# Kernel tuning notes

Measured on AMD Instinct MI355X. Metric: run time of the kernel, lower is better.

## Reference

```python
import jax, jax.numpy as jnp
import numpy as np

ALPHA = 0.05  # mixprop alpha
GDEP = 2      # propagation depth

B, C_IN, N, T = 2, 16, 4096, 12
C_OUT = 16


def _row_norm_with_self_loop(A):
    # A <- (A + I); A / rowsum(A)
    A = A + jnp.eye(A.shape[0], dtype=A.dtype)
    return A / A.sum(axis=1, keepdims=True)


def _qadj_mul(Ar, Ai, Aj, Ak, x):
    # quaternion Hamilton product of adjacency quaternion (Ar,Ai,Aj,Ak)
    # with feature quaternion (channel dim split into 4 components).
    # x: [b, c, n, t] with c % 4 == 0
    xr, xi, xj, xk = jnp.split(x, 4, axis=1)  # each [b, c/4, n, t]
    mm = lambda A, v: jnp.einsum('vw,bcwt->bcvt', A, v)
    out_r = mm(Ar, xr) - mm(Ai, xi) - mm(Aj, xj) - mm(Ak, xk)
    out_i = mm(Ar, xi) + mm(Ai, xr) + mm(Aj, xk) - mm(Ak, xj)
    out_j = mm(Ar, xj) - mm(Ai, xk) + mm(Aj, xr) + mm(Ak, xi)
    out_k = mm(Ar, xk) + mm(Ai, xj) - mm(Aj, xi) + mm(Ak, xr)
    return jnp.concatenate([out_r, out_i, out_j, out_k], axis=1)


def _make_quaternion_mul(kernel):
    # kernel: [K, c_in//4, c_out] -> hamilton: [K, c_in, c_out]
    r, i, j, k = jnp.split(kernel, 4, axis=2)  # each [K, c_in//4, c_out//4]
    r2 = jnp.concatenate([r, -i, -j, -k], axis=1)
    i2 = jnp.concatenate([i, r, -k, j], axis=1)
    j2 = jnp.concatenate([j, k, r, -i], axis=1)
    k2 = jnp.concatenate([k, -j, i, r], axis=1)
    return jnp.concatenate([r2, i2, j2, k2], axis=2)  # [K, c_in, c_out]


def setup_inputs() -> dict:
    key = jax.random.key(0)
    ks = jax.random.split(key, 6)
    x = jax.random.normal(ks[0], (B, C_IN, N, T), dtype=jnp.float32)
    adp_r = jax.random.uniform(ks[1], (N, N), dtype=jnp.float32)
    adp_i = jax.random.uniform(ks[2], (N, N), dtype=jnp.float32)
    adp_j = jax.random.uniform(ks[3], (N, N), dtype=jnp.float32)
    adp_k = jax.random.uniform(ks[4], (N, N), dtype=jnp.float32)
    weight = jax.random.normal(ks[5], (GDEP + 1, C_IN // 4, C_OUT), dtype=jnp.float32)
    return {"x": x, "adp_r": adp_r, "adp_i": adp_i, "adp_j": adp_j,
            "adp_k": adp_k, "weight": weight}


def reference(x, adp_r, adp_i, adp_j, adp_k, weight):
    a_r = adp_r  # note: r-component is NOT normalized in the original
    a_i = _row_norm_with_self_loop(adp_i)
    a_j = _row_norm_with_self_loop(adp_j)
    a_k = _row_norm_with_self_loop(adp_k)

    h = x
    out = [h]
    for _ in range(GDEP):
        h = ALPHA * x + (1.0 - ALPHA) * _qadj_mul(a_r, a_i, a_j, a_k, h)
        out.append(h)
    xs = jnp.stack(out, axis=2)  # [b, c_in, gdep+1, n, t]

    hamilton = _make_quaternion_mul(weight)  # [gdep+1, c_in, c_out]
    return jnp.einsum('bikht,kij->bjht', xs, hamilton)  # [b, c_out, n, t]
```

## Files before the change

### kernel.cpp

```cpp
#include <hip/hip_runtime.h>

typedef __attribute__((ext_vector_type(8))) short short8;
typedef __attribute__((ext_vector_type(4))) float f32x4;

#define ALPHA_F 0.05f

static __device__ __forceinline__ unsigned short f2bf(float f) {
  unsigned int u = __float_as_uint(f);
  unsigned int r = (u + 0x7fffu + ((u >> 16) & 1u)) >> 16;
  return (unsigned short)r;
}

static __device__ __forceinline__ void gld16(const void* g, void* l) {
  __builtin_amdgcn_global_load_lds((const __attribute__((address_space(1))) void*)g,
                                   (__attribute__((address_space(3))) void*)l, 16, 0, 0);
}

__global__ __launch_bounds__(256) void prep_adj(const float* __restrict__ ar,
    const float* __restrict__ ai, const float* __restrict__ aj, const float* __restrict__ ak,
    unsigned short* __restrict__ Abf)
{
  const int bid = blockIdx.x;
  const int p = bid >> 12;
  const int row = bid & 4095;
  const float* src = (p == 0) ? ar : (p == 1) ? ai : (p == 2) ? aj : ak;
  const float4* r4 = (const float4*)(src + ((size_t)row << 12));
  ushort4* dst = (ushort4*)(Abf + (((size_t)p << 12) + (size_t)row) * 4096);

  if (p == 0) {
    for (int i = threadIdx.x; i < 1024; i += 256) {
      float4 v = r4[i];
      dst[i] = make_ushort4(f2bf(v.x), f2bf(v.y), f2bf(v.z), f2bf(v.w));
    }
  } else {
    float4 vals[4];
    float s = 0.f;
    #pragma unroll
    for (int it = 0; it < 4; ++it) {
      float4 v = r4[threadIdx.x + it * 256];
      vals[it] = v;
      s += v.x + v.y + v.z + v.w;
    }
    #pragma unroll
    for (int off = 32; off >= 1; off >>= 1) s += __shfl_down(s, off, 64);
    __shared__ float red[4];
    if ((threadIdx.x & 63) == 0) red[threadIdx.x >> 6] = s;
    __syncthreads();
    const float inv = 1.0f / (red[0] + red[1] + red[2] + red[3] + 1.0f);
    #pragma unroll
    for (int it = 0; it < 4; ++it) {
      const int i = threadIdx.x + it * 256;
      float4 v = vals[it];
      const int base = i << 2;
      if (row - base >= 0 && row - base < 4) ((float*)&v)[row - base] += 1.0f;
      dst[i] = make_ushort4(f2bf(v.x * inv), f2bf(v.y * inv), f2bf(v.z * inv), f2bf(v.w * inv));
    }
  }
}

__global__ __launch_bounds__(256) void pack_x(const float* __restrict__ x,
                                              unsigned short* __restrict__ XT)
{
  __shared__ float tile[3072];
  const int nt = blockIdx.x & 15;
  const int c  = (blockIdx.x >> 4) & 15;
  const int b  = blockIdx.x >> 8;
  const int n0 = nt << 8;
  const int col0 = c * 24 + b * 12;
  const size_t base = ((size_t)(b * 16 + c) * 4096 + n0) * 12;
  #pragma unroll
  for (int it = 0; it < 12; ++it) {
    const int idx = it * 256 + threadIdx.x;
    tile[idx] = x[base + idx];
  }
  __syncthreads();
  #pragma unroll
  for (int it = 0; it < 12; ++it) {
    const int idx = it * 256 + threadIdx.x;
    const int t = idx >> 8, i = idx & 255;
    XT[(size_t)(col0 + t) * 4096 + (n0 + i)] = f2bf(tile[i * 12 + t]);
  }
}

#define SBM 64
#define SBN 384
#define SBK 64

__global__ __launch_bounds__(512, 2) void gemm_p(const unsigned short* __restrict__ A,
    const unsigned short* __restrict__ BT, float* __restrict__ P)
{
  __shared__ __align__(16) unsigned short As[2][SBM * SBK];
  __shared__ __align__(16) unsigned short Bs[2][SBN * SBK];
  const int tid = threadIdx.x;
  const int p  = blockIdx.x >> 6;
  const int n0 = (blockIdx.x & 63) << 6;
  const int lane = tid & 63;
  const int w = tid >> 6;
  const int wm = w >> 2;
  const int ws = w & 3;

  f32x4 acc[2][6];
  #pragma unroll
  for (int m = 0; m < 2; ++m)
    #pragma unroll
    for (int n = 0; n < 6; ++n) acc[m][n] = (f32x4){0.f, 0.f, 0.f, 0.f};

  auto stage = [&](int buf, int kt) {
    const int k0 = kt << 6;
    #pragma unroll
    for (int it = 0; it < 7; ++it) {
      const int idx = it * 512 + tid;
      if (it == 0) {
        const int row = idx >> 3, ch = idx & 7;
        const int chs = ch ^ (row & 7);
        gld16(A + (((size_t)(p * 4096 + n0 + row)) << 12) + (size_t)(k0 + chs * 8),
              (unsigned short*)As[buf] + idx * 8);
      } else {
        const int bidx = idx - 512;
        const int row = bidx >> 3, ch = bidx & 7;
        const int chs = ch ^ (row & 7);
        gld16(BT + ((size_t)row << 12) + (size_t)(k0 + chs * 8),
              (unsigned short*)Bs[buf] + bidx * 8);
      }
    }
  };

  stage(0, 0);
  const int l15 = lane & 15, lk = lane >> 4;
  const int NK = 64;
  for (int kt = 0; kt < NK; ++kt) {
    const int buf = kt & 1;
    if (kt + 1 < NK) {
      stage(buf ^ 1, kt + 1);
      asm volatile("s_waitcnt vmcnt(7)" ::: "memory");
    } else {
      asm volatile("s_waitcnt vmcnt(0)" ::: "memory");
    }
    __builtin_amdgcn_s_barrier();
    __builtin_amdgcn_sched_barrier(0);

    short8 af[2][2], bf[6][2];
    #pragma unroll
    for (int m = 0; m < 2; ++m) {
      const int row = wm * 32 + m * 16 + l15;
      #pragma unroll
      for (int ks = 0; ks < 2; ++ks) {
        const int ck = (lk + ks * 4) ^ (row & 7);
        af[m][ks] = *(const short8*)&As[buf][row * 64 + ck * 8];
      }
    }
    #pragma unroll
    for (int n = 0; n < 6; ++n) {
      const int row = ws * 96 + n * 16 + l15;
      #pragma unroll
      for (int ks = 0; ks < 2; ++ks) {
        const int ck = (lk + ks * 4) ^ (row & 7);
        bf[n][ks] = *(const short8*)&Bs[buf][row * 64 + ck * 8];
      }
    }
    __builtin_amdgcn_s_setprio(1);
    #pragma unroll
    for (int ks = 0; ks < 2; ++ks)
      #pragma unroll
      for (int m = 0; m < 2; ++m)
        #pragma unroll
        for (int n = 0; n < 6; ++n)
          acc[m][n] = __builtin_amdgcn_mfma_f32_16x16x32_bf16(af[m][ks], bf[n][ks], acc[m][n], 0, 0, 0);
    __builtin_amdgcn_s_setprio(0);
    __builtin_amdgcn_sched_barrier(0);
    __builtin_amdgcn_s_barrier();
  }

  float* Pp = P + ((size_t)p * 4096 + (size_t)n0) * 384;
  #pragma unroll
  for (int m = 0; m < 2; ++m) {
    const int r0 = wm * 32 + m * 16 + ((lane >> 4) << 2);
    #pragma unroll
    for (int n = 0; n < 6; ++n) {
      const int cc = ws * 96 + n * 16 + (lane & 15);
      #pragma unroll
      for (int e = 0; e < 4; ++e)
        Pp[(size_t)(r0 + e) * 384 + cc] = acc[m][n][e];
    }
  }
}

__global__ __launch_bounds__(256) void combine_k(const float* __restrict__ P,
    const float* __restrict__ x, float* __restrict__ H, unsigned short* __restrict__ XT,
    const int writeXT)
{
  __shared__ unsigned short T[64][72];
  const int n0 = (blockIdx.x / 6) << 6;
  const int c0 = (blockIdx.x % 6) << 6;
  static const int   sigma_t[4][4] = {{0,1,2,3},{1,0,3,2},{2,3,0,1},{3,2,1,0}};
  static const float sgn_t[4][4]   = {{1,-1,-1,-1},{1,1,1,-1},{1,-1,1,1},{1,1,-1,1}};
  #pragma unroll
  for (int r = 0; r < 16; ++r) {
    const int idx = r * 256 + threadIdx.x;
    const int ln = idx >> 6, lc = idx & 63;
    const int n = n0 + ln, col = c0 + lc;
    const int q = col / 96;
    const int cm = col - q * 96;
    float acc = 0.f;
    #pragma unroll
    for (int p = 0; p < 4; ++p)
      acc += sgn_t[q][p] * P[((size_t)p * 4096 + (size_t)n) * 384 + (size_t)(sigma_t[q][p] * 96 + cm)];
    const int c = col / 24, rr = col - c * 24;
    const int b = rr / 12, t = rr - b * 12;
    const float xv = x[(((size_t)(b * 16 + c) << 12) | (size_t)n) * 12 + t];
    const float h = ALPHA_F * xv + (1.f - ALPHA_F) * acc;
    H[(size_t)n * 384 + col] = h;
    T[lc][ln] = f2bf(h);
  }
  if (writeXT) {
    __syncthreads();
    #pragma unroll
    for (int r = 0; r < 16; ++r) {
      const int idx = r * 256 + threadIdx.x;
      const int lc = idx >> 6, ln = idx & 63;
      XT[((size_t)(c0 + lc) << 12) + (size_t)(n0 + ln)] = T[lc][ln];
    }
  }
}

__global__ __launch_bounds__(256) void final_k(const float* __restrict__ x,
    const float* __restrict__ H1, const float* __restrict__ H2,
    const float* __restrict__ wgt, float* __restrict__ out)
{
  __shared__ float Hm[3][16][16];
  static const int   comp_t[4][4] = {{0,1,2,3},{1,0,3,2},{2,3,0,1},{3,2,1,0}};
  static const float hsgn_t[4][4] = {{1,-1,-1,-1},{1,1,-1,1},{1,1,1,-1},{1,-1,1,1}};
  for (int idx = threadIdx.x; idx < 768; idx += 256) {
    const int k = idx >> 8, i = (idx >> 4) & 15, j = idx & 15;
    const int J = j >> 2, I = i >> 2, a = i & 3, jj = j & 3;
    Hm[k][i][j] = hsgn_t[J][I] * wgt[(k * 4 + a) * 16 + comp_t[J][I] * 4 + jj];
  }
  __syncthreads();
  const int o = blockIdx.x * 256 + threadIdx.x;
  const int t = o % 12;
  const int nb = o / 12;
  const int n = nb & 4095;
  const int b = nb >> 12;
  float v[3][16];
  #pragma unroll
  for (int i = 0; i < 16; ++i)
    v[0][i] = x[((((size_t)(b * 16 + i)) << 12) | (size_t)n) * 12 + t];
  const int colbase = b * 12 + t;
  #pragma unroll
  for (int i = 0; i < 16; ++i) {
    const size_t hidx = (size_t)n * 384 + (size_t)(i * 24 + colbase);
    v[1][i] = H1[hidx];
    v[2][i] = H2[hidx];
  }
  #pragma unroll
  for (int j = 0; j < 16; ++j) {
    float acc = 0.f;
    #pragma unroll
    for (int k = 0; k < 3; ++k)
      #pragma unroll
      for (int i = 0; i < 16; ++i)
        acc += v[k][i] * Hm[k][i][j];
    out[((((size_t)(b * 16 + j)) << 12) | (size_t)n) * 12 + t] = acc;
  }
}

extern "C" void kernel_launch(void* const* d_in, const int* in_sizes, int n_in,
                              void* d_out, int out_size, void* d_ws, size_t ws_size,
                              hipStream_t stream)
{
  const float* x   = (const float*)d_in[0];
  const float* ar  = (const float*)d_in[1];
  const float* ai  = (const float*)d_in[2];
  const float* aj  = (const float*)d_in[3];
  const float* ak  = (const float*)d_in[4];
  const float* wgt = (const float*)d_in[5];
  float* out = (float*)d_out;

  char* ws = (char*)d_ws;
  unsigned short* Abf = (unsigned short*)(ws);
  unsigned short* XT0 = (unsigned short*)(ws + 134217728);
  unsigned short* XT1 = (unsigned short*)(ws + 137363456);
  float*          P   = (float*)(ws + 140509184);
  float*          H1  = (float*)(ws + 165675008);
  float*          H2  = (float*)(ws + 171966464);

  prep_adj<<<dim3(16384), dim3(256), 0, stream>>>(ar, ai, aj, ak, Abf);
  pack_x<<<dim3(512), dim3(256), 0, stream>>>(x, XT0);
  gemm_p<<<dim3(256), dim3(512), 0, stream>>>(Abf, XT0, P);
  combine_k<<<dim3(384), dim3(256), 0, stream>>>(P, x, H1, XT1, 1);
  gemm_p<<<dim3(256), dim3(512), 0, stream>>>(Abf, XT1, P);
  combine_k<<<dim3(384), dim3(256), 0, stream>>>(P, x, H2, XT1, 0);
  final_k<<<dim3(384), dim3(256), 0, stream>>>(x, H1, H2, wgt, out);
}
```

Baseline: 506.9 us.

## Split-K GEMM with 128x192 tiles and one-wave-per-row adjacency prep

The adjacency GEMM is retiled from 64x384 blocks to 128x192 output tiles with a 2-way split over K, giving 512 blocks instead of 256 for better occupancy. Partial sums go to a doubled P buffer that combine_k now reduces over 8 slices, and the workspace offsets are shifted to make room. prep_adj assigns one wavefront per row and uses shuffle-xor reductions instead of block-level LDS reductions. The costs are extra P traffic, the split-K reduction, and some duplicated B loads from clamped rows.

Result: slower. 591.4 us (+16.7%).

```diff
diff --git a/kernel.cpp b/kernel.cpp
--- a/kernel.cpp
+++ b/kernel.cpp
@@ -20,41 +20,41 @@
     const float* __restrict__ ai, const float* __restrict__ aj, const float* __restrict__ ak,
     unsigned short* __restrict__ Abf)
 {
-  const int bid = blockIdx.x;
-  const int p = bid >> 12;
-  const int row = bid & 4095;
+  const int w = threadIdx.x >> 6, lane = threadIdx.x & 63;
+  const int wid = blockIdx.x * 4 + w;
+  const int p = wid >> 12;
+  const int row = wid & 4095;
   const float* src = (p == 0) ? ar : (p == 1) ? ai : (p == 2) ? aj : ak;
   const float4* r4 = (const float4*)(src + ((size_t)row << 12));
-  ushort4* dst = (ushort4*)(Abf + (((size_t)p << 12) + (size_t)row) * 4096);
+  ushort4* dst = (ushort4*)(Abf + ((size_t)wid << 12));
+
+  float4 v[16];
+  #pragma unroll
+  for (int i = 0; i < 16; ++i) v[i] = r4[lane + i * 64];
 
   if (p == 0) {
-    for (int i = threadIdx.x; i < 1024; i += 256) {
-      float4 v = r4[i];
-      dst[i] = make_ushort4(f2bf(v.x), f2bf(v.y), f2bf(v.z), f2bf(v.w));
-    }
+    #pragma unroll
+    for (int i = 0; i < 16; ++i)
+      dst[lane + i * 64] = make_ushort4(f2bf(v[i].x), f2bf(v[i].y), f2bf(v[i].z), f2bf(v[i].w));
   } else {
-    float4 vals[4];
     float s = 0.f;
     #pragma unroll
-    for (int it = 0; it < 4; ++it) {
-      float4 v = r4[threadIdx.x + it * 256];
-      vals[it] = v;
-      s += v.x + v.y + v.z + v.w;
-    }
-    #pragma unroll
-    for (int off = 32; off >= 1; off >>= 1) s += __shfl_down(s, off, 64);
-    __shared__ float red[4];
-    if ((threadIdx.x & 63) == 0) red[threadIdx.x >> 6] = s;
-    __syncthreads();
-    const float inv = 1.0f / (red[0] + red[1] + red[2] + red[3] + 1.0f);
-    #pragma unroll
-    for (int it = 0; it < 4; ++it) {
-      const int i = threadIdx.x + it * 256;
-      float4 v = vals[it];
-      const int base = i << 2;
-      if (row - base >= 0 && row - base < 4) ((float*)&v)[row - base] += 1.0f;
-      dst[i] = make_ushort4(f2bf(v.x * inv), f2bf(v.y * inv), f2bf(v.z * inv), f2bf(v.w * inv));
-    }
+    for (int i = 0; i < 16; ++i) s += v[i].x + v[i].y + v[i].z + v[i].w;
+    #pragma unroll
+    for (int off = 1; off < 64; off <<= 1) s += __shfl_xor(s, off, 64);
+    const float inv = 1.0f / (s + 1.0f);
+    #pragma unroll
+    for (int i = 0; i < 16; ++i) {
+      const int base = (i * 64 + lane) << 2;
+      v[i].x += (base + 0 == row) ? 1.0f : 0.0f;
+      v[i].y += (base + 1 == row) ? 1.0f : 0.0f;
+      v[i].z += (base + 2 == row) ? 1.0f : 0.0f;
+      v[i].w += (base + 3 == row) ? 1.0f : 0.0f;
+    }
+    #pragma unroll
+    for (int i = 0; i < 16; ++i)
+      dst[lane + i * 64] = make_ushort4(f2bf(v[i].x * inv), f2bf(v[i].y * inv),
+                                        f2bf(v[i].z * inv), f2bf(v[i].w * inv));
   }
 }
 
@@ -82,46 +82,44 @@
   }
 }
 
-#define SBM 64
-#define SBN 384
-#define SBK 64
-
-__global__ __launch_bounds__(512, 2) void gemm_p(const unsigned short* __restrict__ A,
+__global__ __launch_bounds__(512, 4) void gemm_p(const unsigned short* __restrict__ A,
     const unsigned short* __restrict__ BT, float* __restrict__ P)
 {
-  __shared__ __align__(16) unsigned short As[2][SBM * SBK];
-  __shared__ __align__(16) unsigned short Bs[2][SBN * SBK];
+  __shared__ __align__(16) unsigned short As[2][512 * 8];
+  __shared__ __align__(16) unsigned short Bs[2][1024 * 8];
   const int tid = threadIdx.x;
-  const int p  = blockIdx.x >> 6;
-  const int n0 = (blockIdx.x & 63) << 6;
+  const int bx = blockIdx.x;
+  const int p  = bx & 3;
+  const int nt = (bx >> 2) & 1;
+  const int kh = (bx >> 3) & 1;
+  const int m0 = (bx >> 4) << 7;
+  const int n0 = nt * 192;
+  const int kbase = kh * 2048;
   const int lane = tid & 63;
   const int w = tid >> 6;
   const int wm = w >> 2;
   const int ws = w & 3;
 
-  f32x4 acc[2][6];
-  #pragma unroll
-  for (int m = 0; m < 2; ++m)
-    #pragma unroll
-    for (int n = 0; n < 6; ++n) acc[m][n] = (f32x4){0.f, 0.f, 0.f, 0.f};
+  f32x4 acc[4][3];
+  #pragma unroll
+  for (int m = 0; m < 4; ++m)
+    #pragma unroll
+    for (int n = 0; n < 3; ++n) acc[m][n] = (f32x4){0.f, 0.f, 0.f, 0.f};
 
   auto stage = [&](int buf, int kt) {
-    const int k0 = kt << 6;
-    #pragma unroll
-    for (int it = 0; it < 7; ++it) {
-      const int idx = it * 512 + tid;
-      if (it == 0) {
-        const int row = idx >> 3, ch = idx & 7;
-        const int chs = ch ^ (row & 7);
-        gld16(A + (((size_t)(p * 4096 + n0 + row)) << 12) + (size_t)(k0 + chs * 8),
-              (unsigned short*)As[buf] + idx * 8);
-      } else {
-        const int bidx = idx - 512;
-        const int row = bidx >> 3, ch = bidx & 7;
-        const int chs = ch ^ (row & 7);
-        gld16(BT + ((size_t)row << 12) + (size_t)(k0 + chs * 8),
-              (unsigned short*)Bs[buf] + bidx * 8);
-      }
+    const int k0 = kbase + (kt << 5);
+    {
+      const int row = tid & 127, ch = tid >> 7;
+      gld16(A + (((size_t)(p * 4096 + m0 + row)) << 12) + (size_t)(k0 + ch * 8),
+            (unsigned short*)As[buf] + tid * 8);
+    }
+    #pragma unroll
+    for (int it = 0; it < 2; ++it) {
+      const int bidx = it * 512 + tid;
+      const int row = bidx & 255, ch = bidx >> 8;
+      const int grow = n0 + (row < 192 ? row : 191);
+      gld16(BT + ((size_t)grow << 12) + (size_t)(k0 + ch * 8),
+            (unsigned short*)Bs[buf] + bidx * 8);
     }
   };
 
@@ -132,52 +130,42 @@
     const int buf = kt & 1;
     if (kt + 1 < NK) {
       stage(buf ^ 1, kt + 1);
-      asm volatile("s_waitcnt vmcnt(7)" ::: "memory");
+      asm volatile("s_waitcnt vmcnt(3)" ::: "memory");
     } else {
       asm volatile("s_waitcnt vmcnt(0)" ::: "memory");
     }
     __builtin_amdgcn_s_barrier();
     __builtin_amdgcn_sched_barrier(0);
 
-    short8 af[2][2], bf[6][2];
-    #pragma unroll
-    for (int m = 0; m < 2; ++m) {
-      const int row = wm * 32 + m * 16 + l15;
+    short8 af[4], bfr[3];
+    #pragma unroll
+    for (int m = 0; m < 4; ++m) {
+      const int row = wm * 64 + m * 16 + l15;
+      af[m] = *(const short8*)&As[buf][(lk * 128 + row) * 8];
+    }
+    #pragma unroll
+    for (int n = 0; n < 3; ++n) {
+      const int row = ws * 48 + n * 16 + l15;
+      bfr[n] = *(const short8*)&Bs[buf][(lk * 256 + row) * 8];
+    }
+    __builtin_amdgcn_s_setprio(1);
+    #pragma unroll
+    for (int m = 0; m < 4; ++m)
       #pragma unroll
-      for (int ks = 0; ks < 2; ++ks) {
-        const int ck = (lk + ks * 4) ^ (row & 7);
-        af[m][ks] = *(const short8*)&As[buf][row * 64 + ck * 8];
-      }
-    }
-    #pragma unroll
-    for (int n = 0; n < 6; ++n) {
-      const int row = ws * 96 + n * 16 + l15;
-      #pragma unroll
-      for (int ks = 0; ks < 2; ++ks) {
-        const int ck = (lk + ks * 4) ^ (row & 7);
-        bf[n][ks] = *(const short8*)&Bs[buf][row * 64 + ck * 8];
-      }
-    }
-    __builtin_amdgcn_s_setprio(1);
-    #pragma unroll
-    for (int ks = 0; ks < 2; ++ks)
-      #pragma unroll
-      for (int m = 0; m < 2; ++m)
-        #pragma unroll
-        for (int n = 0; n < 6; ++n)
-          acc[m][n] = __builtin_amdgcn_mfma_f32_16x16x32_bf16(af[m][ks], bf[n][ks], acc[m][n], 0, 0, 0);
+      for (int n = 0; n < 3; ++n)
+        acc[m][n] = __builtin_amdgcn_mfma_f32_16x16x32_bf16(af[m], bfr[n], acc[m][n], 0, 0, 0);
     __builtin_amdgcn_s_setprio(0);
     __builtin_amdgcn_sched_barrier(0);
     __builtin_amdgcn_s_barrier();
   }
 
-  float* Pp = P + ((size_t)p * 4096 + (size_t)n0) * 384;
-  #pragma unroll
-  for (int m = 0; m < 2; ++m) {
-    const int r0 = wm * 32 + m * 16 + ((lane >> 4) << 2);
-    #pragma unroll
-    for (int n = 0; n < 6; ++n) {
-      const int cc = ws * 96 + n * 16 + (lane & 15);
+  float* Pp = P + (((size_t)(kh * 4 + p) * 4096 + m0) * 384);
+  #pragma unroll
+  for (int m = 0; m < 4; ++m) {
+    const int r0 = wm * 64 + m * 16 + lk * 4;
+    #pragma unroll
+    for (int n = 0; n < 3; ++n) {
+      const int cc = n0 + ws * 48 + n * 16 + l15;
       #pragma unroll
       for (int e = 0; e < 4; ++e)
         Pp[(size_t)(r0 + e) * 384 + cc] = acc[m][n][e];
@@ -203,8 +191,10 @@
     const int cm = col - q * 96;
     float acc = 0.f;
     #pragma unroll
-    for (int p = 0; p < 4; ++p)
-      acc += sgn_t[q][p] * P[((size_t)p * 4096 + (size_t)n) * 384 + (size_t)(sigma_t[q][p] * 96 + cm)];
+    for (int pp = 0; pp < 8; ++pp) {
+      const int p4 = pp & 3;
+      acc += sgn_t[q][p4] * P[((size_t)pp * 4096 + (size_t)n) * 384 + (size_t)(sigma_t[q][p4] * 96 + cm)];
+    }
     const int c = col / 24, rr = col - c * 24;
     const int b = rr / 12, t = rr - b * 12;
     const float xv = x[(((size_t)(b * 16 + c) << 12) | (size_t)n) * 12 + t];
@@ -281,14 +271,14 @@
   unsigned short* XT0 = (unsigned short*)(ws + 134217728);
   unsigned short* XT1 = (unsigned short*)(ws + 137363456);
   float*          P   = (float*)(ws + 140509184);
-  float*          H1  = (float*)(ws + 165675008);
-  float*          H2  = (float*)(ws + 171966464);
-
-  prep_adj<<<dim3(16384), dim3(256), 0, stream>>>(ar, ai, aj, ak, Abf);
+  float*          H1  = (float*)(ws + 190840832);
+  float*          H2  = (float*)(ws + 197132288);
+
+  prep_adj<<<dim3(4096), dim3(256), 0, stream>>>(ar, ai, aj, ak, Abf);
   pack_x<<<dim3(512), dim3(256), 0, stream>>>(x, XT0);
-  gemm_p<<<dim3(256), dim3(512), 0, stream>>>(Abf, XT0, P);
+  gemm_p<<<dim3(512), dim3(512), 0, stream>>>(Abf, XT0, P);
   combine_k<<<dim3(384), dim3(256), 0, stream>>>(P, x, H1, XT1, 1);
-  gemm_p<<<dim3(256), dim3(512), 0, stream>>>(Abf, XT1, P);
+  gemm_p<<<dim3(512), dim3(512), 0, stream>>>(Abf, XT1, P);
   combine_k<<<dim3(384), dim3(256), 0, stream>>>(P, x, H2, XT1, 0);
   final_k<<<dim3(384), dim3(256), 0, stream>>>(x, H1, H2, wgt, out);
 }
```
